# Kernel tuning notes

Hardware: AMD Instinct MI355X
Metric: run time of the kernel (lower is better)

## Reference

```python
import jax, jax.numpy as jnp
import numpy as np

N = 50000          # nodes
E = 500000         # edges (avg degree 10)
WIDTH = 128        # node feature width
HID = 128          # width * scale, scale=1 -> 2 heads of 64
HEAD = 64          # head_dim (module-level constant)
EMB = WIDTH // 2   # edge-embed width = 64
RES = 1.0
BOND = (5, 6, 2, 17)  # bond_size vocabularies


def setup_inputs() -> dict:
    key = jax.random.key(0)
    ks = jax.random.split(key, 24)
    w = lambda k, s: (jax.random.normal(k, s, jnp.float32) * 0.02)
    inp = {
        "x": jax.random.normal(ks[0], (N, WIDTH), jnp.float32),
        "edge_index": jax.random.randint(ks[1], (2, E), 0, N),
        "edge_attr": jax.random.randint(ks[2], (E, 4), 0, 3),
        # pre: Linear(width, width)
        "pre_w": w(ks[3], (WIDTH, WIDTH)), "pre_b": jnp.zeros((WIDTH,), jnp.float32),
        # msg[0..3]: Linear(width, hidden)
        "msg0_w": w(ks[4], (WIDTH, HID)), "msg0_b": jnp.zeros((HID,), jnp.float32),
        "msg1_w": w(ks[5], (WIDTH, HID)), "msg1_b": jnp.zeros((HID,), jnp.float32),
        "msg2_w": w(ks[6], (WIDTH, HID)), "msg2_b": jnp.zeros((HID,), jnp.float32),
        "msg3_w": w(ks[7], (WIDTH, HID)), "msg3_b": jnp.zeros((HID,), jnp.float32),
        # remix[0..2]: Linear(width//2, hidden)
        "remix0_w": w(ks[8], (EMB, HID)), "remix0_b": jnp.zeros((HID,), jnp.float32),
        "remix1_w": w(ks[9], (EMB, HID)), "remix1_b": jnp.zeros((HID,), jnp.float32),
        "remix2_w": w(ks[10], (EMB, HID)), "remix2_b": jnp.zeros((HID,), jnp.float32),
        # post: Linear(hidden, width)
        "post_w": w(ks[11], (HID, WIDTH)), "post_b": jnp.zeros((WIDTH,), jnp.float32),
        # EmbedBlock tables (bond_size + 1 rows each); tables 1..3 have padding_idx=0
        "emb0": w(ks[12], (BOND[0] + 1, EMB)),
        "emb1": w(ks[13], (BOND[1] + 1, EMB)).at[0].set(0.0),
        "emb2": w(ks[14], (BOND[2] + 1, EMB)).at[0].set(0.0),
        "emb3": w(ks[15], (BOND[3] + 1, EMB)).at[0].set(0.0),
        "einit": jnp.zeros((4,), jnp.float32),          # EmbedBlock.init0
        "init0": jnp.zeros((4,), jnp.float32),          # ConvBlock.init0 (hop*2+2)
    }
    return inp


def _gelu(v):
    return jax.nn.gelu(v, approximate=False)


def _ln(v):
    m = jnp.mean(v, axis=-1, keepdims=True)
    var = jnp.mean(jnp.square(v - m), axis=-1, keepdims=True)
    return (v - m) / jnp.sqrt(var + 1e-5)


def reference(x, edge_index, edge_attr, pre_w, pre_b, msg0_w, msg0_b,
              msg1_w, msg1_b, msg2_w, msg2_b, msg3_w, msg3_b,
              remix0_w, remix0_b, remix1_w, remix1_b, remix2_w, remix2_b,
              post_w, post_b, emb0, emb1, emb2, emb3, einit, init0):
    n = x.shape[0]
    e = edge_index.shape[1]
    xx = _ln(x @ pre_w + pre_b)  # pre: Linear + LayerNorm(no affine)
    # EmbedBlock: weighted sum of per-column embeddings, xw = exp(a)/sqrt(sum exp(a))
    xw = jnp.exp(einit) / jnp.sqrt(jnp.sum(jnp.exp(einit)))
    ee = (emb0[edge_attr[:, 0]] * xw[0] + emb1[edge_attr[:, 1]] * xw[1]
          + emb2[edge_attr[:, 2]] * xw[2] + emb3[edge_attr[:, 3]] * xw[3])  # [E, 64]
    src, dst = edge_index[0], edge_index[1]  # source_to_target: j=src, i=dst
    x_j = xx[src]
    x_i = xx[dst]
    scale_e = jnp.exp(init0[-2])
    scale_v = jnp.exp(init0[-1])
    q = x_i @ msg1_w + msg1_b + (ee @ remix0_w + remix0_b) * scale_e  # [E, HID]
    k = x_j @ msg2_w + msg2_b + (ee @ remix1_w + remix1_b) * scale_e
    v = _gelu(x_j @ msg3_w + msg3_b + (ee @ remix2_w + remix2_b) * scale_v)
    # per-head attention score, head_dim = 64
    att = jnp.sum((q * k).reshape(e, -1, HEAD), axis=-1, keepdims=True) / np.sqrt(HEAD)
    att = jnp.exp(att * init0[0] + init0[1])  # edge_type=0, hop=1
    msg = (v.reshape(e, -1, HEAD) * att).reshape(e, -1)  # [E, HID]
    agg = jax.ops.segment_sum(msg, dst, num_segments=n)  # scatter-add to targets
    xx = _gelu(xx @ msg0_w + msg0_b) + agg
    out = xx @ post_w + post_b
    return x + out * RES
```

## Files before the change

kernel.cpp:

```cpp
#include <hip/hip_runtime.h>
#include <cstdint>

#define WIDTH 128
#define NCOMBO 2268
#define XSL 136
#define OSL 132
#define TOTW (6 * 16384)
#define TOTU (3 * 34 * WIDTH)

typedef short bf16x8 __attribute__((ext_vector_type(8)));
typedef float f32x4  __attribute__((ext_vector_type(4)));

__device__ __forceinline__ float gelu_fast(float v) {
    float e = __builtin_amdgcn_exp2f(v * __builtin_fmaf(v * v, 0.1029437f, 2.3022081f));
    return v - v * __builtin_amdgcn_rcpf(e + 1.0f);
}
__device__ __forceinline__ short f2b(float f) {
    unsigned u = __float_as_uint(f);
    unsigned r = (u + 0x7FFFu + ((u >> 16) & 1u)) >> 16;
    return (short)r;
}
__device__ __forceinline__ float b2f_lo(unsigned u) { return __uint_as_float(u << 16); }
__device__ __forceinline__ float b2f_hi(unsigned u) { return __uint_as_float(u & 0xFFFF0000u); }
__device__ __forceinline__ unsigned pack2(float lo, float hi) {
    return (unsigned)(unsigned short)f2b(lo) | ((unsigned)(unsigned short)f2b(hi) << 16);
}

__global__ void k_f1(const float* __restrict__ einit, const float* __restrict__ init0,
                     const float* __restrict__ emb0, const float* __restrict__ emb1,
                     const float* __restrict__ emb2, const float* __restrict__ emb3,
                     const float* __restrict__ r0w, const float* __restrict__ r0b,
                     const float* __restrict__ r1w, const float* __restrict__ r1b,
                     const float* __restrict__ r2w, const float* __restrict__ r2b,
                     const float* __restrict__ pw0, const float* __restrict__ pw1,
                     const float* __restrict__ pw2, const float* __restrict__ pw3,
                     const float* __restrict__ pw4, const float* __restrict__ pw5,
                     short* __restrict__ o0, short* __restrict__ o1,
                     short* __restrict__ o2, short* __restrict__ o3,
                     short* __restrict__ o4, short* __restrict__ o5,
                     float* __restrict__ U, float* __restrict__ scal,
                     const int* __restrict__ edge_index, int* __restrict__ counts,
                     int* __restrict__ rank, int* __restrict__ done, int E) {
    int tid = blockIdx.x * blockDim.x + threadIdx.x;
    if (tid == 0) { scal[0] = init0[0]; scal[1] = init0[1]; done[0] = 0; }
    if (tid < TOTW) {
        int which = tid >> 14;
        int r = tid & 16383;
        int t    = r >> 11;
        int kc   = (r >> 9) & 3;
        int lane = (r >> 3) & 63;
        int j    = r & 7;
        int k  = kc * 32 + ((lane >> 4) << 3) + j;
        int nn = (t << 4) + (lane & 15);
        const float* w = (which == 0) ? pw0 : (which == 1) ? pw1 : (which == 2) ? pw2
                       : (which == 3) ? pw3 : (which == 4) ? pw4 : pw5;
        short* o = (which == 0) ? o0 : (which == 1) ? o1 : (which == 2) ? o2
                 : (which == 3) ? o3 : (which == 4) ? o4 : o5;
        o[r] = f2b(w[k * 128 + nn]);
    } else if (tid < TOTW + TOTU) {
        int idx = tid - TOTW;
        float e0 = expf(einit[0]), e1 = expf(einit[1]), e2 = expf(einit[2]), e3 = expf(einit[3]);
        float inv = 1.0f / sqrtf(e0 + e1 + e2 + e3);
        float xw[4] = {e0 * inv, e1 * inv, e2 * inv, e3 * inv};
        float se = expf(init0[2]);
        float sv = expf(init0[3]);
        int r   = idx / (34 * WIDTH);
        int rem = idx - r * (34 * WIDTH);
        int g   = rem / WIDTH;
        int j   = rem - g * WIDTH;
        int cc, base;
        if (g >= 16)      { cc = 3; base = 16; }
        else if (g >= 13) { cc = 2; base = 13; }
        else if (g >= 6)  { cc = 1; base = 6; }
        else              { cc = 0; base = 0; }
        int i = g - base;
        const float* em = (cc == 0) ? emb0 : (cc == 1) ? emb1 : (cc == 2) ? emb2 : emb3;
        const float* w  = (r == 0) ? r0w : (r == 1) ? r1w : r2w;
        const float* rb = (r == 0) ? r0b : (r == 1) ? r1b : r2b;
        float s = (r == 2) ? sv : se;
        float acc = 0.0f;
        const float* erow = em + i * 64;
        for (int d = 0; d < 64; ++d) acc += erow[d] * w[d * WIDTH + j];
        float val = s * xw[cc] * acc;
        if (cc == 0) val += s * rb[j];
        U[idx] = val;
    } else if (tid < TOTW + TOTU + E) {
        int e = tid - TOTW - TOTU;
        rank[e] = atomicAdd(&counts[edge_index[E + e]], 1);
    }
}

__global__ void k_f2(const int* __restrict__ counts, int* __restrict__ lscan,
                     int* __restrict__ partials, int n, int sb,
                     const float* __restrict__ U, const float* __restrict__ init0,
                     float* __restrict__ Uc, int* __restrict__ done,
                     int* __restrict__ offsets) {
    if ((int)blockIdx.x < sb) {
        __shared__ int s[256];
        __shared__ int flag;
        int t = threadIdx.x;
        int i = blockIdx.x * 256 + t;
        int v = (i < n) ? counts[i] : 0;
        s[t] = v;
        __syncthreads();
        for (int d = 1; d < 256; d <<= 1) {
            int u = (t >= d) ? s[t - d] : 0;
            __syncthreads();
            s[t] += u;
            __syncthreads();
        }
        if (i < n) lscan[i] = s[t];
        if (t == 255) atomicExch(&partials[blockIdx.x], s[255]);
        __syncthreads();
        if (t == 0) {
            __threadfence();
            flag = (atomicAdd(done, 1) == sb - 1);
        }
        __syncthreads();
        if (flag) {
            __threadfence();
            int b0 = t * 4;
            int a0 = (b0     < sb) ? partials[b0]     : 0;
            int a1 = (b0 + 1 < sb) ? partials[b0 + 1] : 0;
            int a2 = (b0 + 2 < sb) ? partials[b0 + 2] : 0;
            int a3 = (b0 + 3 < sb) ? partials[b0 + 3] : 0;
            int tsum = a0 + a1 + a2 + a3;
            __syncthreads();
            s[t] = tsum;
            __syncthreads();
            for (int d = 1; d < 256; d <<= 1) {
                int u = (t >= d) ? s[t - d] : 0;
                __syncthreads();
                s[t] += u;
                __syncthreads();
            }
            int excl = s[t] - tsum;
            if (b0     < sb) partials[b0]     = excl;
            if (b0 + 1 < sb) partials[b0 + 1] = excl + a0;
            if (b0 + 2 < sb) partials[b0 + 2] = excl + a0 + a1;
            if (b0 + 3 < sb) partials[b0 + 3] = excl + a0 + a1 + a2;
            if (t == 255) offsets[n] = s[255];
        }
    } else {
        int bi = ((int)blockIdx.x - sb) * 2 + (threadIdx.x >> 7);
        if (bi >= 3 * NCOMBO) return;
        int r  = bi / NCOMBO;
        if (r < 2 && init0[0] == 0.0f) return;
        int cb = bi - r * NCOMBO;
        int a  = cb / 378;
        int rm = cb - a * 378;
        int b  = rm / 54;
        rm -= b * 54;
        int c  = rm / 18;
        int d  = rm - c * 18;
        int j  = threadIdx.x & 127;
        const float* Ur = U + r * 34 * WIDTH;
        Uc[(size_t)bi * WIDTH + j] = Ur[a * WIDTH + j] + Ur[(6 + b) * WIDTH + j]
                                   + Ur[(13 + c) * WIDTH + j] + Ur[(16 + d) * WIDTH + j];
    }
}

__global__ void __launch_bounds__(256, 2) k_f3(
        const float* __restrict__ x,
        const short* __restrict__ preF, const float* __restrict__ pre_b,
        const short* __restrict__ w0F, const float* __restrict__ b0,
        const short* __restrict__ w1F, const float* __restrict__ b1,
        const short* __restrict__ w2F, const float* __restrict__ b2,
        const short* __restrict__ w3F, const float* __restrict__ b3,
        const float* __restrict__ scal,
        short* __restrict__ Gb, float* __restrict__ A,
        short* __restrict__ Bb, short* __restrict__ Cb, int n,
        const int* __restrict__ edge_index, const int* __restrict__ edge_attr,
        const int* __restrict__ counts, const int* __restrict__ lscan,
        const int* __restrict__ partials, const int* __restrict__ rank,
        int* __restrict__ offsets, unsigned* __restrict__ s_pk, int E,
        int gb, int eb) {
    __shared__ short xs_raw[64 * XSL];
    __shared__ short xs_xx[64 * XSL];
    int tid = threadIdx.x;

    if ((int)blockIdx.x >= gb) {
        int rb = (int)blockIdx.x - gb;
        if (rb < eb) {
            int e = rb * 256 + tid;
            if (e >= E) return;
            int src = edge_index[e];
            int dst = edge_index[E + e];
            int4 at = ((const int4*)edge_attr)[e];
            int combo = ((at.x * 7 + at.y) * 3 + at.z) * 18 + at.w;
            int off = partials[dst >> 8] + lscan[dst] - counts[dst];
            s_pk[off + rank[e]] = (unsigned)src | ((unsigned)combo << 17);
        } else {
            int i = (rb - eb) * 256 + tid;
            if (i >= n) return;
            offsets[i] = partials[i >> 8] + lscan[i] - counts[i];
        }
        return;
    }

    int w    = tid >> 6;
    int lane = tid & 63;
    int quad = lane >> 4, l16 = lane & 15;
    int m0   = blockIdx.x * 64;

    bf16x8 Bg[2][4], Bc[2][4];
#pragma unroll
    for (int tt = 0; tt < 2; ++tt)
#pragma unroll
        for (int kc = 0; kc < 4; ++kc) {
            int fo = (((2 * w + tt) * 4 + kc) * 64 + lane) * 8;
            Bg[tt][kc] = *(const bf16x8*)(w0F + fo);
            Bc[tt][kc] = *(const bf16x8*)(w3F + fo);
        }

#pragma unroll
    for (int it = 0; it < 8; ++it) {
        int fi  = it * 256 + tid;
        int row = fi >> 5, c4 = fi & 31;
        int gr  = min(m0 + row, n - 1);
        float4 v = ((const float4*)x)[(size_t)gr * 32 + c4];
        uint2 p;
        p.x = pack2(v.x, v.y);
        p.y = pack2(v.z, v.w);
        *(uint2*)(&xs_raw[row * XSL + c4 * 4]) = p;
    }
    __syncthreads();

    {
        bf16x8 a[4];
#pragma unroll
        for (int kc = 0; kc < 4; ++kc)
            a[kc] = *(const bf16x8*)(&xs_raw[(w * 16 + l16) * XSL + kc * 32 + quad * 8]);
        f32x4 acc[8];
#pragma unroll
        for (int t = 0; t < 8; ++t) acc[t] = (f32x4){0.f, 0.f, 0.f, 0.f};
#pragma unroll
        for (int kc = 0; kc < 4; ++kc)
#pragma unroll
            for (int t = 0; t < 8; ++t) {
                bf16x8 b = *(const bf16x8*)(preF + ((t * 4 + kc) * 64 + lane) * 8);
                acc[t] = __builtin_amdgcn_mfma_f32_16x16x32_bf16(a[kc], b, acc[t], 0, 0, 0);
            }
#pragma unroll
        for (int t = 0; t < 8; ++t) {
            float bv = pre_b[t * 16 + l16];
#pragma unroll
            for (int r = 0; r < 4; ++r) acc[t][r] += bv;
        }
#pragma unroll
        for (int r = 0; r < 4; ++r) {
            float s = 0.f, s2 = 0.f;
#pragma unroll
            for (int t = 0; t < 8; ++t) { float v = acc[t][r]; s += v; s2 += v * v; }
            s  += __shfl_xor(s, 1);  s2 += __shfl_xor(s2, 1);
            s  += __shfl_xor(s, 2);  s2 += __shfl_xor(s2, 2);
            s  += __shfl_xor(s, 4);  s2 += __shfl_xor(s2, 4);
            s  += __shfl_xor(s, 8);  s2 += __shfl_xor(s2, 8);
            float m   = s * (1.0f / WIDTH);
            float var = s2 * (1.0f / WIDTH) - m * m;
            float rs  = rsqrtf(var + 1e-5f);
#pragma unroll
            for (int t = 0; t < 8; ++t) acc[t][r] = (acc[t][r] - m) * rs;
        }
        int rowb = w * 16 + quad * 4;
#pragma unroll
        for (int t = 0; t < 8; ++t)
#pragma unroll
            for (int r = 0; r < 4; ++r)
                xs_xx[(rowb + r) * XSL + t * 16 + l16] = f2b(acc[t][r]);
    }
    __syncthreads();

    bf16x8 a2[4][4];
#pragma unroll
    for (int i = 0; i < 4; ++i)
#pragma unroll
        for (int kc = 0; kc < 4; ++kc)
            a2[i][kc] = *(const bf16x8*)(&xs_xx[(i * 16 + l16) * XSL + kc * 32 + quad * 8]);
    __syncthreads();

    {
        f32x4 accG[4][2], accC[4][2];
#pragma unroll
        for (int i = 0; i < 4; ++i)
#pragma unroll
            for (int tt = 0; tt < 2; ++tt) {
                accG[i][tt] = (f32x4){0.f,0.f,0.f,0.f};
                accC[i][tt] = (f32x4){0.f,0.f,0.f,0.f};
            }
#pragma unroll
        for (int kc = 0; kc < 4; ++kc)
#pragma unroll
            for (int i = 0; i < 4; ++i)
#pragma unroll
                for (int tt = 0; tt < 2; ++tt) {
                    accG[i][tt] = __builtin_amdgcn_mfma_f32_16x16x32_bf16(a2[i][kc], Bg[tt][kc], accG[i][tt], 0, 0, 0);
                    accC[i][tt] = __builtin_amdgcn_mfma_f32_16x16x32_bf16(a2[i][kc], Bc[tt][kc], accC[i][tt], 0, 0, 0);
                }
#pragma unroll
        for (int tt = 0; tt < 2; ++tt) {
            int col = (2 * w + tt) * 16 + l16;
            float bg = b0[col];
            float bc = b3[col];
#pragma unroll
            for (int i = 0; i < 4; ++i)
#pragma unroll
                for (int r = 0; r < 4; ++r) {
                    int row = i * 16 + quad * 4 + r;
                    xs_raw[row * XSL + col] = f2b(gelu_fast(accG[i][tt][r] + bg));
                    xs_xx[row * XSL + col]  = f2b(accC[i][tt][r] + bc);
                }
        }
    }
    __syncthreads();

#pragma unroll
    for (int it = 0; it < 4; ++it) {
        int si  = it * 256 + tid;
        int row = si >> 4, c8 = si & 15;
        if (m0 + row < n) {
            *(bf16x8*)(Gb + (size_t)(m0 + row) * WIDTH + c8 * 8) = *(const bf16x8*)(&xs_raw[row * XSL + c8 * 8]);
            *(bf16x8*)(Cb + (size_t)(m0 + row) * WIDTH + c8 * 8) = *(const bf16x8*)(&xs_xx[row * XSL + c8 * 8]);
        }
    }

    if (scal[0] != 0.0f) {
        bf16x8 Ba[2][4], Bbf[2][4];
#pragma unroll
        for (int tt = 0; tt < 2; ++tt)
#pragma unroll
            for (int kc = 0; kc < 4; ++kc) {
                int fo = (((2 * w + tt) * 4 + kc) * 64 + lane) * 8;
                Ba[tt][kc]  = *(const bf16x8*)(w1F + fo);
                Bbf[tt][kc] = *(const bf16x8*)(w2F + fo);
            }
        f32x4 accA[4][2], accB[4][2];
#pragma unroll
        for (int i = 0; i < 4; ++i)
#pragma unroll
            for (int tt = 0; tt < 2; ++tt) {
                accA[i][tt] = (f32x4){0.f,0.f,0.f,0.f};
                accB[i][tt] = (f32x4){0.f,0.f,0.f,0.f};
            }
#pragma unroll
        for (int kc = 0; kc < 4; ++kc)
#pragma unroll
            for (int i = 0; i < 4; ++i)
#pragma unroll
                for (int tt = 0; tt < 2; ++tt) {
                    accA[i][tt] = __builtin_amdgcn_mfma_f32_16x16x32_bf16(a2[i][kc], Ba[tt][kc],  accA[i][tt], 0, 0, 0);
                    accB[i][tt] = __builtin_amdgcn_mfma_f32_16x16x32_bf16(a2[i][kc], Bbf[tt][kc], accB[i][tt], 0, 0, 0);
                }
#pragma unroll
        for (int tt = 0; tt < 2; ++tt) {
            int col = (2 * w + tt) * 16 + l16;
            float ba = b1[col];
            float bb = b2[col];
#pragma unroll
            for (int i = 0; i < 4; ++i)
#pragma unroll
                for (int r = 0; r < 4; ++r) {
                    int row = m0 + i * 16 + quad * 4 + r;
                    if (row < n) {
                        size_t idx = (size_t)row * WIDTH + col;
                        A[idx]  = accA[i][tt][r] + ba;
                        Bb[idx] = f2b(accB[i][tt][r] + bb);
                    }
                }
        }
    }
}

__global__ void __launch_bounds__(256)
k_agg(const int* __restrict__ offsets, const unsigned* __restrict__ s_pk,
      const float* __restrict__ A, const short* __restrict__ Bb,
      const short* __restrict__ Cb, const float* __restrict__ Uc,
      const float* __restrict__ scal, const short* __restrict__ Gb,
      short* __restrict__ hb, int n) {
    int wid = threadIdx.x >> 6;
    int L   = threadIdx.x & 63;
    int node = blockIdx.x * 4 + wid;
    if (node >= n) return;
    int start = __builtin_amdgcn_readfirstlane(offsets[node]);
    int end   = __builtin_amdgcn_readfirstlane(offsets[node + 1]);

    const unsigned* Cb32 = (const unsigned*)Cb;
    const unsigned* Bb32 = (const unsigned*)Bb;
    const float2* U0c2 = (const float2*)(Uc);
    const float2* U1c2 = (const float2*)(Uc + (size_t)NCOMBO * WIDTH);
    const float2* U2c2 = (const float2*)(Uc + 2 * (size_t)NCOMBO * WIDTH);

    float i0 = scal[0], i1 = scal[1];
    float acc0 = 0.0f, acc1 = 0.0f;

    if (i0 == 0.0f) {
        int p = start;
        for (; p + 4 <= end; p += 4) {
            unsigned pk0 = __builtin_amdgcn_readfirstlane(s_pk[p]);
            unsigned pk1 = __builtin_amdgcn_readfirstlane(s_pk[p + 1]);
            unsigned pk2 = __builtin_amdgcn_readfirstlane(s_pk[p + 2]);
            unsigned pk3 = __builtin_amdgcn_readfirstlane(s_pk[p + 3]);
            const unsigned* cp0 = Cb32 + ((size_t)(pk0 & 0x1FFFFu) << 6);
            const unsigned* cp1 = Cb32 + ((size_t)(pk1 & 0x1FFFFu) << 6);
            const unsigned* cp2 = Cb32 + ((size_t)(pk2 & 0x1FFFFu) << 6);
            const unsigned* cp3 = Cb32 + ((size_t)(pk3 & 0x1FFFFu) << 6);
            const float2* up0 = U2c2 + ((size_t)(pk0 >> 17) << 6);
            const float2* up1 = U2c2 + ((size_t)(pk1 >> 17) << 6);
            const float2* up2 = U2c2 + ((size_t)(pk2 >> 17) << 6);
            const float2* up3 = U2c2 + ((size_t)(pk3 >> 17) << 6);
            unsigned cc0 = cp0[L], cc1 = cp1[L], cc2 = cp2[L], cc3 = cp3[L];
            float2   uu0 = up0[L], uu1 = up1[L], uu2 = up2[L], uu3 = up3[L];
            acc0 += gelu_fast(b2f_lo(cc0) + uu0.x);
            acc1 += gelu_fast(b2f_hi(cc0) + uu0.y);
            acc0 += gelu_fast(b2f_lo(cc1) + uu1.x);
            acc1 += gelu_fast(b2f_hi(cc1) + uu1.y);
            acc0 += gelu_fast(b2f_lo(cc2) + uu2.x);
            acc1 += gelu_fast(b2f_hi(cc2) + uu2.y);
            acc0 += gelu_fast(b2f_lo(cc3) + uu3.x);
            acc1 += gelu_fast(b2f_hi(cc3) + uu3.y);
        }
        if (p + 2 <= end) {
            unsigned pk0 = __builtin_amdgcn_readfirstlane(s_pk[p]);
            unsigned pk1 = __builtin_amdgcn_readfirstlane(s_pk[p + 1]);
            const unsigned* cp0 = Cb32 + ((size_t)(pk0 & 0x1FFFFu) << 6);
            const unsigned* cp1 = Cb32 + ((size_t)(pk1 & 0x1FFFFu) << 6);
            const float2* up0 = U2c2 + ((size_t)(pk0 >> 17) << 6);
            const float2* up1 = U2c2 + ((size_t)(pk1 >> 17) << 6);
            unsigned cc0 = cp0[L], cc1 = cp1[L];
            float2   uu0 = up0[L], uu1 = up1[L];
            acc0 += gelu_fast(b2f_lo(cc0) + uu0.x);
            acc1 += gelu_fast(b2f_hi(cc0) + uu0.y);
            acc0 += gelu_fast(b2f_lo(cc1) + uu1.x);
            acc1 += gelu_fast(b2f_hi(cc1) + uu1.y);
            p += 2;
        }
        if (p < end) {
            unsigned pk0 = __builtin_amdgcn_readfirstlane(s_pk[p]);
            const unsigned* cp0 = Cb32 + ((size_t)(pk0 & 0x1FFFFu) << 6);
            const float2* up0 = U2c2 + ((size_t)(pk0 >> 17) << 6);
            unsigned cc0 = cp0[L];
            float2   uu0 = up0[L];
            acc0 += gelu_fast(b2f_lo(cc0) + uu0.x);
            acc1 += gelu_fast(b2f_hi(cc0) + uu0.y);
        }
        float sE = __expf(i1);
        acc0 *= sE; acc1 *= sE;
    } else {
        float2 av = *(const float2*)(A + (size_t)node * WIDTH + 2 * L);
        int p = start;
        for (; p + 2 <= end; p += 2) {
            unsigned pk0 = s_pk[p], pk1 = s_pk[p + 1];
            unsigned sA = pk0 & 0x1FFFFu, cA = pk0 >> 17;
            unsigned sB = pk1 & 0x1FFFFu, cB = pk1 >> 17;
            float2 u0a = U0c2[cA * 64 + L], u0b = U0c2[cB * 64 + L];
            float2 u1a = U1c2[cA * 64 + L], u1b = U1c2[cB * 64 + L];
            float2 u2a = U2c2[cA * 64 + L], u2b = U2c2[cB * 64 + L];
            unsigned bba = Bb32[sA * 64 + L], bbb = Bb32[sB * 64 + L];
            unsigned cca = Cb32[sA * 64 + L], ccb = Cb32[sB * 64 + L];
            {
                float q0 = av.x + u0a.x, q1 = av.y + u0a.y;
                float k0 = b2f_lo(bba) + u1a.x, k1 = b2f_hi(bba) + u1a.y;
                float v0 = gelu_fast(b2f_lo(cca) + u2a.x);
                float v1 = gelu_fast(b2f_hi(cca) + u2a.y);
                float s = q0 * k0 + q1 * k1;
                s += __shfl_xor(s, 1);
                s += __shfl_xor(s, 2);
                s += __shfl_xor(s, 4);
                s += __shfl_xor(s, 8);
                s += __shfl_xor(s, 16);
                float att = __expf(s * 0.125f * i0 + i1);
                acc0 += v0 * att;
                acc1 += v1 * att;
            }
            {
                float q0 = av.x + u0b.x, q1 = av.y + u0b.y;
                float k0 = b2f_lo(bbb) + u1b.x, k1 = b2f_hi(bbb) + u1b.y;
                float v0 = gelu_fast(b2f_lo(ccb) + u2b.x);
                float v1 = gelu_fast(b2f_hi(ccb) + u2b.y);
                float s = q0 * k0 + q1 * k1;
                s += __shfl_xor(s, 1);
                s += __shfl_xor(s, 2);
                s += __shfl_xor(s, 4);
                s += __shfl_xor(s, 8);
                s += __shfl_xor(s, 16);
                float att = __expf(s * 0.125f * i0 + i1);
                acc0 += v0 * att;
                acc1 += v1 * att;
            }
        }
        if (p < end) {
            unsigned pk = s_pk[p];
            unsigned sA = pk & 0x1FFFFu, cA = pk >> 17;
            float2 u0 = U0c2[cA * 64 + L];
            float2 u1 = U1c2[cA * 64 + L];
            float2 u2 = U2c2[cA * 64 + L];
            unsigned bb = Bb32[sA * 64 + L];
            unsigned cc = Cb32[sA * 64 + L];
            float q0 = av.x + u0.x, q1 = av.y + u0.y;
            float k0 = b2f_lo(bb) + u1.x, k1 = b2f_hi(bb) + u1.y;
            float v0 = gelu_fast(b2f_lo(cc) + u2.x);
            float v1 = gelu_fast(b2f_hi(cc) + u2.y);
            float s = q0 * k0 + q1 * k1;
            s += __shfl_xor(s, 1);
            s += __shfl_xor(s, 2);
            s += __shfl_xor(s, 4);
            s += __shfl_xor(s, 8);
            s += __shfl_xor(s, 16);
            float att = __expf(s * 0.125f * i0 + i1);
            acc0 += v0 * att;
            acc1 += v1 * att;
        }
    }
    unsigned g = ((const unsigned*)Gb)[(size_t)node * 64 + L];
    ((unsigned*)hb)[(size_t)node * 64 + L] = pack2(b2f_lo(g) + acc0, b2f_hi(g) + acc1);
}

__global__ void __launch_bounds__(256, 2) k_post(
        const float* __restrict__ x, const short* __restrict__ hb,
        const short* __restrict__ postF, const float* __restrict__ post_b,
        float* __restrict__ out, int n) {
    __shared__ short hs[64 * XSL];
    __shared__ float os[64 * OSL];
    int tid  = threadIdx.x;
    int w    = tid >> 6;
    int lane = tid & 63;
    int quad = lane >> 4, l16 = lane & 15;
    int m0   = blockIdx.x * 64;

    bf16x8 Bp[2][4];
#pragma unroll
    for (int tt = 0; tt < 2; ++tt)
#pragma unroll
        for (int kc = 0; kc < 4; ++kc)
            Bp[tt][kc] = *(const bf16x8*)(postF + (((2 * w + tt) * 4 + kc) * 64 + lane) * 8);

#pragma unroll
    for (int it = 0; it < 4; ++it) {
        int si  = it * 256 + tid;
        int row = si >> 4, c8 = si & 15;
        int gr  = min(m0 + row, n - 1);
        *(bf16x8*)(&hs[row * XSL + c8 * 8]) = *(const bf16x8*)(hb + (size_t)gr * WIDTH + c8 * 8);
    }
    __syncthreads();

    bf16x8 a[4][4];
#pragma unroll
    for (int i = 0; i < 4; ++i)
#pragma unroll
        for (int kc = 0; kc < 4; ++kc)
            a[i][kc] = *(const bf16x8*)(&hs[(i * 16 + l16) * XSL + kc * 32 + quad * 8]);

    f32x4 acc[4][2];
#pragma unroll
    for (int i = 0; i < 4; ++i)
#pragma unroll
        for (int tt = 0; tt < 2; ++tt) acc[i][tt] = (f32x4){0.f,0.f,0.f,0.f};
#pragma unroll
    for (int kc = 0; kc < 4; ++kc)
#pragma unroll
        for (int i = 0; i < 4; ++i)
#pragma unroll
            for (int tt = 0; tt < 2; ++tt)
                acc[i][tt] = __builtin_amdgcn_mfma_f32_16x16x32_bf16(a[i][kc], Bp[tt][kc], acc[i][tt], 0, 0, 0);

#pragma unroll
    for (int tt = 0; tt < 2; ++tt) {
        int col = (2 * w + tt) * 16 + l16;
        float bv = post_b[col];
#pragma unroll
        for (int i = 0; i < 4; ++i)
#pragma unroll
            for (int r = 0; r < 4; ++r)
                os[(i * 16 + quad * 4 + r) * OSL + col] = acc[i][tt][r] + bv;
    }
    __syncthreads();

#pragma unroll
    for (int it = 0; it < 8; ++it) {
        int fi  = it * 256 + tid;
        int row = fi >> 5, c4 = fi & 31;
        if (m0 + row < n) {
            float4 xv = ((const float4*)x)[(size_t)(m0 + row) * 32 + c4];
            float4 av = *(const float4*)(&os[row * OSL + c4 * 4]);
            float4 ov = {xv.x + av.x, xv.y + av.y, xv.z + av.z, xv.w + av.w};
            ((float4*)out)[(size_t)(m0 + row) * 32 + c4] = ov;
        }
    }
}

extern "C" void kernel_launch(void* const* d_in, const int* in_sizes, int n_in,
                              void* d_out, int out_size, void* d_ws, size_t ws_size,
                              hipStream_t stream) {
    const float* x      = (const float*)d_in[0];
    const int*   eidx   = (const int*)d_in[1];
    const int*   eattr  = (const int*)d_in[2];
    const float* pre_w  = (const float*)d_in[3];
    const float* pre_b  = (const float*)d_in[4];
    const float* msg0_w = (const float*)d_in[5];
    const float* msg0_b = (const float*)d_in[6];
    const float* msg1_w = (const float*)d_in[7];
    const float* msg1_b = (const float*)d_in[8];
    const float* msg2_w = (const float*)d_in[9];
    const float* msg2_b = (const float*)d_in[10];
    const float* msg3_w = (const float*)d_in[11];
    const float* msg3_b = (const float*)d_in[12];
    const float* r0w    = (const float*)d_in[13];
    const float* r0b    = (const float*)d_in[14];
    const float* r1w    = (const float*)d_in[15];
    const float* r1b    = (const float*)d_in[16];
    const float* r2w    = (const float*)d_in[17];
    const float* r2b    = (const float*)d_in[18];
    const float* post_w = (const float*)d_in[19];
    const float* post_b = (const float*)d_in[20];
    const float* emb0   = (const float*)d_in[21];
    const float* emb1   = (const float*)d_in[22];
    const float* emb2   = (const float*)d_in[23];
    const float* emb3   = (const float*)d_in[24];
    const float* einit  = (const float*)d_in[25];
    const float* init0  = (const float*)d_in[26];

    int n = in_sizes[0] / WIDTH;
    int E = in_sizes[2] / 4;
    size_t NW = (size_t)n * WIDTH;

    float* ws   = (float*)d_ws;
    float* A    = ws;
    float* U    = ws + NW;
    float* Uc   = U + 3 * 34 * WIDTH;
    float* scal = Uc + 3 * (size_t)NCOMBO * WIDTH;
    short* sw   = (short*)(scal + 2);
    short* preF  = sw;
    short* w0F   = sw + 16384;
    short* w1F   = sw + 2 * 16384;
    short* w2F   = sw + 3 * 16384;
    short* w3F   = sw + 4 * 16384;
    short* postF = sw + 5 * 16384;
    short* Bb    = sw + 6 * 16384;
    short* Cb    = Bb + NW;
    short* Gb    = Cb + NW;
    short* hb    = Gb + NW;
    int*      ib       = (int*)(hb + NW);
    int*      offsets  = ib;
    int*      counts   = offsets + (n + 1);
    int*      lscan    = counts + n;
    int*      partials = lscan + n;
    int*      rank     = partials + 1024;
    unsigned* s_pk     = (unsigned*)(rank + E);
    int*      done     = (int*)(s_pk + E);

    hipMemsetAsync(counts, 0, (size_t)n * sizeof(int), stream);

    int f1_total = TOTW + TOTU + E;
    k_f1<<<(f1_total + 255) / 256, 256, 0, stream>>>(
        einit, init0, emb0, emb1, emb2, emb3,
        r0w, r0b, r1w, r1b, r2w, r2b,
        pre_w, msg0_w, msg1_w, msg2_w, msg3_w, post_w,
        preF, w0F, w1F, w2F, w3F, postF, U, scal,
        eidx, counts, rank, done, E);

    int sb  = (n + 255) / 256;
    int pcb = (3 * NCOMBO + 1) / 2;
    k_f2<<<sb + pcb, 256, 0, stream>>>(counts, lscan, partials, n, sb, U, init0, Uc,
                                       done, offsets);

    int gb = (n + 63) / 64;
    int eb = (E + 255) / 256;
    k_f3<<<gb + eb + sb, 256, 0, stream>>>(
        x, preF, pre_b, w0F, msg0_b, w1F, msg1_b, w2F, msg2_b, w3F, msg3_b,
        scal, Gb, A, Bb, Cb, n,
        eidx, eattr, counts, lscan, partials, rank, offsets, s_pk, E, gb, eb);

    k_agg<<<(n + 3) / 4, 256, 0, stream>>>(offsets, s_pk, A, Bb, Cb, Uc, scal, Gb, hb, n);
    k_post<<<gb, 256, 0, stream>>>(x, hb, postF, post_b, (float*)d_out, n);
}
```

Baseline: 232.9 us.

## Fuse edge aggregation into post projection kernel via shared-memory tile

Merges the per-node aggregation kernel and the post linear kernel into one kernel. Each 512-thread block aggregates 32 nodes (four per wave) into a bf16 tile in LDS, then runs the MFMA post projection and residual add directly on it. This removes the hb global round trip and one launch. It also loads edge descriptors 64 at a time with one vector load and reads them with readlane instead of per-edge scalar loads. In exchange, each wave walks four nodes in sequence, blocks wait at a barrier for their slowest node, and post weights are reloaded per block with smaller MFMA tiles.

```diff
diff --git a/kernel.cpp b/kernel.cpp
--- a/kernel.cpp
+++ b/kernel.cpp
@@ -371,213 +371,139 @@
     }
 }
 
-__global__ void __launch_bounds__(256)
-k_agg(const int* __restrict__ offsets, const unsigned* __restrict__ s_pk,
-      const float* __restrict__ A, const short* __restrict__ Bb,
-      const short* __restrict__ Cb, const float* __restrict__ Uc,
-      const float* __restrict__ scal, const short* __restrict__ Gb,
-      short* __restrict__ hb, int n) {
-    int wid = threadIdx.x >> 6;
-    int L   = threadIdx.x & 63;
-    int node = blockIdx.x * 4 + wid;
-    if (node >= n) return;
-    int start = __builtin_amdgcn_readfirstlane(offsets[node]);
-    int end   = __builtin_amdgcn_readfirstlane(offsets[node + 1]);
+__global__ void __launch_bounds__(512, 6)
+k_ap(const int* __restrict__ offsets, const unsigned* __restrict__ s_pk,
+     const float* __restrict__ A, const short* __restrict__ Bb,
+     const short* __restrict__ Cb, const float* __restrict__ Uc,
+     const float* __restrict__ scal, const short* __restrict__ Gb,
+     const float* __restrict__ x, const short* __restrict__ postF,
+     const float* __restrict__ post_b, float* __restrict__ out, int n) {
+    __shared__ short hs[32 * XSL];
+    __shared__ float os[32 * OSL];
+    int tid = threadIdx.x;
+    int w   = tid >> 6;
+    int L   = tid & 63;
+    int m0  = blockIdx.x * 32;
 
     const unsigned* Cb32 = (const unsigned*)Cb;
     const unsigned* Bb32 = (const unsigned*)Bb;
     const float2* U0c2 = (const float2*)(Uc);
     const float2* U1c2 = (const float2*)(Uc + (size_t)NCOMBO * WIDTH);
     const float2* U2c2 = (const float2*)(Uc + 2 * (size_t)NCOMBO * WIDTH);
+    unsigned* hs32 = (unsigned*)hs;
 
     float i0 = scal[0], i1 = scal[1];
-    float acc0 = 0.0f, acc1 = 0.0f;
-
-    if (i0 == 0.0f) {
-        int p = start;
-        for (; p + 4 <= end; p += 4) {
-            unsigned pk0 = __builtin_amdgcn_readfirstlane(s_pk[p]);
-            unsigned pk1 = __builtin_amdgcn_readfirstlane(s_pk[p + 1]);
-            unsigned pk2 = __builtin_amdgcn_readfirstlane(s_pk[p + 2]);
-            unsigned pk3 = __builtin_amdgcn_readfirstlane(s_pk[p + 3]);
-            const unsigned* cp0 = Cb32 + ((size_t)(pk0 & 0x1FFFFu) << 6);
-            const unsigned* cp1 = Cb32 + ((size_t)(pk1 & 0x1FFFFu) << 6);
-            const unsigned* cp2 = Cb32 + ((size_t)(pk2 & 0x1FFFFu) << 6);
-            const unsigned* cp3 = Cb32 + ((size_t)(pk3 & 0x1FFFFu) << 6);
-            const float2* up0 = U2c2 + ((size_t)(pk0 >> 17) << 6);
-            const float2* up1 = U2c2 + ((size_t)(pk1 >> 17) << 6);
-            const float2* up2 = U2c2 + ((size_t)(pk2 >> 17) << 6);
-            const float2* up3 = U2c2 + ((size_t)(pk3 >> 17) << 6);
-            unsigned cc0 = cp0[L], cc1 = cp1[L], cc2 = cp2[L], cc3 = cp3[L];
-            float2   uu0 = up0[L], uu1 = up1[L], uu2 = up2[L], uu3 = up3[L];
-            acc0 += gelu_fast(b2f_lo(cc0) + uu0.x);
-            acc1 += gelu_fast(b2f_hi(cc0) + uu0.y);
-            acc0 += gelu_fast(b2f_lo(cc1) + uu1.x);
-            acc1 += gelu_fast(b2f_hi(cc1) + uu1.y);
-            acc0 += gelu_fast(b2f_lo(cc2) + uu2.x);
-            acc1 += gelu_fast(b2f_hi(cc2) + uu2.y);
-            acc0 += gelu_fast(b2f_lo(cc3) + uu3.x);
-            acc1 += gelu_fast(b2f_hi(cc3) + uu3.y);
-        }
-        if (p + 2 <= end) {
-            unsigned pk0 = __builtin_amdgcn_readfirstlane(s_pk[p]);
-            unsigned pk1 = __builtin_amdgcn_readfirstlane(s_pk[p + 1]);
-            const unsigned* cp0 = Cb32 + ((size_t)(pk0 & 0x1FFFFu) << 6);
-            const unsigned* cp1 = Cb32 + ((size_t)(pk1 & 0x1FFFFu) << 6);
-            const float2* up0 = U2c2 + ((size_t)(pk0 >> 17) << 6);
-            const float2* up1 = U2c2 + ((size_t)(pk1 >> 17) << 6);
-            unsigned cc0 = cp0[L], cc1 = cp1[L];
-            float2   uu0 = up0[L], uu1 = up1[L];
-            acc0 += gelu_fast(b2f_lo(cc0) + uu0.x);
-            acc1 += gelu_fast(b2f_hi(cc0) + uu0.y);
-            acc0 += gelu_fast(b2f_lo(cc1) + uu1.x);
-            acc1 += gelu_fast(b2f_hi(cc1) + uu1.y);
-            p += 2;
-        }
-        if (p < end) {
-            unsigned pk0 = __builtin_amdgcn_readfirstlane(s_pk[p]);
-            const unsigned* cp0 = Cb32 + ((size_t)(pk0 & 0x1FFFFu) << 6);
-            const float2* up0 = U2c2 + ((size_t)(pk0 >> 17) << 6);
-            unsigned cc0 = cp0[L];
-            float2   uu0 = up0[L];
-            acc0 += gelu_fast(b2f_lo(cc0) + uu0.x);
-            acc1 += gelu_fast(b2f_hi(cc0) + uu0.y);
-        }
-        float sE = __expf(i1);
-        acc0 *= sE; acc1 *= sE;
-    } else {
-        float2 av = *(const float2*)(A + (size_t)node * WIDTH + 2 * L);
-        int p = start;
-        for (; p + 2 <= end; p += 2) {
-            unsigned pk0 = s_pk[p], pk1 = s_pk[p + 1];
-            unsigned sA = pk0 & 0x1FFFFu, cA = pk0 >> 17;
-            unsigned sB = pk1 & 0x1FFFFu, cB = pk1 >> 17;
-            float2 u0a = U0c2[cA * 64 + L], u0b = U0c2[cB * 64 + L];
-            float2 u1a = U1c2[cA * 64 + L], u1b = U1c2[cB * 64 + L];
-            float2 u2a = U2c2[cA * 64 + L], u2b = U2c2[cB * 64 + L];
-            unsigned bba = Bb32[sA * 64 + L], bbb = Bb32[sB * 64 + L];
-            unsigned cca = Cb32[sA * 64 + L], ccb = Cb32[sB * 64 + L];
-            {
-                float q0 = av.x + u0a.x, q1 = av.y + u0a.y;
-                float k0 = b2f_lo(bba) + u1a.x, k1 = b2f_hi(bba) + u1a.y;
-                float v0 = gelu_fast(b2f_lo(cca) + u2a.x);
-                float v1 = gelu_fast(b2f_hi(cca) + u2a.y);
-                float s = q0 * k0 + q1 * k1;
-                s += __shfl_xor(s, 1);
-                s += __shfl_xor(s, 2);
-                s += __shfl_xor(s, 4);
-                s += __shfl_xor(s, 8);
-                s += __shfl_xor(s, 16);
-                float att = __expf(s * 0.125f * i0 + i1);
-                acc0 += v0 * att;
-                acc1 += v1 * att;
+    float sE = __expf(i1);
+
+    for (int k = 0; k < 4; ++k) {
+        int row  = w * 4 + k;
+        int node = m0 + row;
+        float acc0 = 0.0f, acc1 = 0.0f;
+        if (node < n) {
+            int start = __builtin_amdgcn_readfirstlane(offsets[node]);
+            int end   = __builtin_amdgcn_readfirstlane(offsets[node + 1]);
+            if (i0 == 0.0f) {
+                for (int base = start; base < end; base += 64) {
+                    int cnt = min(end - base, 64);
+                    unsigned pkv = (L < cnt) ? s_pk[base + L] : 0u;
+                    int i = 0;
+                    for (; i + 4 <= cnt; i += 4) {
+                        unsigned pk0 = __builtin_amdgcn_readlane(pkv, i);
+                        unsigned pk1 = __builtin_amdgcn_readlane(pkv, i + 1);
+                        unsigned pk2 = __builtin_amdgcn_readlane(pkv, i + 2);
+                        unsigned pk3 = __builtin_amdgcn_readlane(pkv, i + 3);
+                        const unsigned* cp0 = Cb32 + ((size_t)(pk0 & 0x1FFFFu) << 6);
+                        const unsigned* cp1 = Cb32 + ((size_t)(pk1 & 0x1FFFFu) << 6);
+                        const unsigned* cp2 = Cb32 + ((size_t)(pk2 & 0x1FFFFu) << 6);
+                        const unsigned* cp3 = Cb32 + ((size_t)(pk3 & 0x1FFFFu) << 6);
+                        const float2* up0 = U2c2 + ((size_t)(pk0 >> 17) << 6);
+                        const float2* up1 = U2c2 + ((size_t)(pk1 >> 17) << 6);
+                        const float2* up2 = U2c2 + ((size_t)(pk2 >> 17) << 6);
+                        const float2* up3 = U2c2 + ((size_t)(pk3 >> 17) << 6);
+                        unsigned cc0 = cp0[L], cc1 = cp1[L], cc2 = cp2[L], cc3 = cp3[L];
+                        float2   uu0 = up0[L], uu1 = up1[L], uu2 = up2[L], uu3 = up3[L];
+                        acc0 += gelu_fast(b2f_lo(cc0) + uu0.x);
+                        acc1 += gelu_fast(b2f_hi(cc0) + uu0.y);
+                        acc0 += gelu_fast(b2f_lo(cc1) + uu1.x);
+                        acc1 += gelu_fast(b2f_hi(cc1) + uu1.y);
+                        acc0 += gelu_fast(b2f_lo(cc2) + uu2.x);
+                        acc1 += gelu_fast(b2f_hi(cc2) + uu2.y);
+                        acc0 += gelu_fast(b2f_lo(cc3) + uu3.x);
+                        acc1 += gelu_fast(b2f_hi(cc3) + uu3.y);
+                    }
+                    for (; i < cnt; ++i) {
+                        unsigned pk0 = __builtin_amdgcn_readlane(pkv, i);
+                        const unsigned* cp0 = Cb32 + ((size_t)(pk0 & 0x1FFFFu) << 6);
+                        const float2* up0 = U2c2 + ((size_t)(pk0 >> 17) << 6);
+                        unsigned cc0 = cp0[L];
+                        float2   uu0 = up0[L];
+                        acc0 += gelu_fast(b2f_lo(cc0) + uu0.x);
+                        acc1 += gelu_fast(b2f_hi(cc0) + uu0.y);
+                    }
+                }
+                acc0 *= sE; acc1 *= sE;
+            } else {
+                float2 av = *(const float2*)(A + (size_t)node * WIDTH + 2 * L);
+                for (int p = start; p < end; ++p) {
+                    unsigned pk = s_pk[p];
+                    unsigned sA = pk & 0x1FFFFu, cA = pk >> 17;
+                    float2 u0 = U0c2[cA * 64 + L];
+                    float2 u1 = U1c2[cA * 64 + L];
+                    float2 u2 = U2c2[cA * 64 + L];
+                    unsigned bb = Bb32[sA * 64 + L];
+                    unsigned cc = Cb32[sA * 64 + L];
+                    float q0 = av.x + u0.x, q1 = av.y + u0.y;
+                    float k0 = b2f_lo(bb) + u1.x, k1 = b2f_hi(bb) + u1.y;
+                    float v0 = gelu_fast(b2f_lo(cc) + u2.x);
+                    float v1 = gelu_fast(b2f_hi(cc) + u2.y);
+                    float s = q0 * k0 + q1 * k1;
+                    s += __shfl_xor(s, 1);
+                    s += __shfl_xor(s, 2);
+                    s += __shfl_xor(s, 4);
+                    s += __shfl_xor(s, 8);
+                    s += __shfl_xor(s, 16);
+                    float att = __expf(s * 0.125f * i0 + i1);
+                    acc0 += v0 * att;
+                    acc1 += v1 * att;
+                }
             }
-            {
-                float q0 = av.x + u0b.x, q1 = av.y + u0b.y;
-                float k0 = b2f_lo(bbb) + u1b.x, k1 = b2f_hi(bbb) + u1b.y;
-                float v0 = gelu_fast(b2f_lo(ccb) + u2b.x);
-                float v1 = gelu_fast(b2f_hi(ccb) + u2b.y);
-                float s = q0 * k0 + q1 * k1;
-                s += __shfl_xor(s, 1);
-                s += __shfl_xor(s, 2);
-                s += __shfl_xor(s, 4);
-                s += __shfl_xor(s, 8);
-                s += __shfl_xor(s, 16);
-                float att = __expf(s * 0.125f * i0 + i1);
-                acc0 += v0 * att;
-                acc1 += v1 * att;
-            }
-        }
-        if (p < end) {
-            unsigned pk = s_pk[p];
-            unsigned sA = pk & 0x1FFFFu, cA = pk >> 17;
-            float2 u0 = U0c2[cA * 64 + L];
-            float2 u1 = U1c2[cA * 64 + L];
-            float2 u2 = U2c2[cA * 64 + L];
-            unsigned bb = Bb32[sA * 64 + L];
-            unsigned cc = Cb32[sA * 64 + L];
-            float q0 = av.x + u0.x, q1 = av.y + u0.y;
-            float k0 = b2f_lo(bb) + u1.x, k1 = b2f_hi(bb) + u1.y;
-            float v0 = gelu_fast(b2f_lo(cc) + u2.x);
-            float v1 = gelu_fast(b2f_hi(cc) + u2.y);
-            float s = q0 * k0 + q1 * k1;
-            s += __shfl_xor(s, 1);
-            s += __shfl_xor(s, 2);
-            s += __shfl_xor(s, 4);
-            s += __shfl_xor(s, 8);
-            s += __shfl_xor(s, 16);
-            float att = __expf(s * 0.125f * i0 + i1);
-            acc0 += v0 * att;
-            acc1 += v1 * att;
-        }
-    }
-    unsigned g = ((const unsigned*)Gb)[(size_t)node * 64 + L];
-    ((unsigned*)hb)[(size_t)node * 64 + L] = pack2(b2f_lo(g) + acc0, b2f_hi(g) + acc1);
-}
-
-__global__ void __launch_bounds__(256, 2) k_post(
-        const float* __restrict__ x, const short* __restrict__ hb,
-        const short* __restrict__ postF, const float* __restrict__ post_b,
-        float* __restrict__ out, int n) {
-    __shared__ short hs[64 * XSL];
-    __shared__ float os[64 * OSL];
-    int tid  = threadIdx.x;
-    int w    = tid >> 6;
-    int lane = tid & 63;
-    int quad = lane >> 4, l16 = lane & 15;
-    int m0   = blockIdx.x * 64;
-
-    bf16x8 Bp[2][4];
-#pragma unroll
-    for (int tt = 0; tt < 2; ++tt)
-#pragma unroll
-        for (int kc = 0; kc < 4; ++kc)
-            Bp[tt][kc] = *(const bf16x8*)(postF + (((2 * w + tt) * 4 + kc) * 64 + lane) * 8);
-
-#pragma unroll
-    for (int it = 0; it < 4; ++it) {
-        int si  = it * 256 + tid;
-        int row = si >> 4, c8 = si & 15;
-        int gr  = min(m0 + row, n - 1);
-        *(bf16x8*)(&hs[row * XSL + c8 * 8]) = *(const bf16x8*)(hb + (size_t)gr * WIDTH + c8 * 8);
+            unsigned g = ((const unsigned*)Gb)[(size_t)node * 64 + L];
+            hs32[row * (XSL / 2) + L] = pack2(b2f_lo(g) + acc0, b2f_hi(g) + acc1);
+        } else {
+            hs32[row * (XSL / 2) + L] = 0u;
+        }
     }
     __syncthreads();
 
-    bf16x8 a[4][4];
-#pragma unroll
-    for (int i = 0; i < 4; ++i)
-#pragma unroll
-        for (int kc = 0; kc < 4; ++kc)
-            a[i][kc] = *(const bf16x8*)(&hs[(i * 16 + l16) * XSL + kc * 32 + quad * 8]);
-
-    f32x4 acc[4][2];
-#pragma unroll
-    for (int i = 0; i < 4; ++i)
-#pragma unroll
-        for (int tt = 0; tt < 2; ++tt) acc[i][tt] = (f32x4){0.f,0.f,0.f,0.f};
+    int quad = L >> 4, l16 = L & 15;
+    int ri    = w & 1;
+    int cpair = w >> 1;
+
+    bf16x8 a[4];
 #pragma unroll
     for (int kc = 0; kc < 4; ++kc)
-#pragma unroll
-        for (int i = 0; i < 4; ++i)
-#pragma unroll
-            for (int tt = 0; tt < 2; ++tt)
-                acc[i][tt] = __builtin_amdgcn_mfma_f32_16x16x32_bf16(a[i][kc], Bp[tt][kc], acc[i][tt], 0, 0, 0);
+        a[kc] = *(const bf16x8*)(&hs[(ri * 16 + l16) * XSL + kc * 32 + quad * 8]);
 
 #pragma unroll
     for (int tt = 0; tt < 2; ++tt) {
-        int col = (2 * w + tt) * 16 + l16;
+        int t = cpair * 2 + tt;
+        f32x4 acc = (f32x4){0.f, 0.f, 0.f, 0.f};
+#pragma unroll
+        for (int kc = 0; kc < 4; ++kc) {
+            bf16x8 b = *(const bf16x8*)(postF + ((t * 4 + kc) * 64 + L) * 8);
+            acc = __builtin_amdgcn_mfma_f32_16x16x32_bf16(a[kc], b, acc, 0, 0, 0);
+        }
+        int col = t * 16 + l16;
         float bv = post_b[col];
 #pragma unroll
-        for (int i = 0; i < 4; ++i)
-#pragma unroll
-            for (int r = 0; r < 4; ++r)
-                os[(i * 16 + quad * 4 + r) * OSL + col] = acc[i][tt][r] + bv;
+        for (int r = 0; r < 4; ++r)
+            os[(ri * 16 + quad * 4 + r) * OSL + col] = acc[r] + bv;
     }
     __syncthreads();
 
 #pragma unroll
-    for (int it = 0; it < 8; ++it) {
-        int fi  = it * 256 + tid;
+    for (int it = 0; it < 2; ++it) {
+        int fi  = it * 512 + tid;
         int row = fi >> 5, c4 = fi & 31;
         if (m0 + row < n) {
             float4 xv = ((const float4*)x)[(size_t)(m0 + row) * 32 + c4];
@@ -638,8 +564,7 @@
     short* Bb    = sw + 6 * 16384;
     short* Cb    = Bb + NW;
     short* Gb    = Cb + NW;
-    short* hb    = Gb + NW;
-    int*      ib       = (int*)(hb + NW);
+    int*      ib       = (int*)(Gb + NW);
     int*      offsets  = ib;
     int*      counts   = offsets + (n + 1);
     int*      lscan    = counts + n;
@@ -670,6 +595,6 @@
         scal, Gb, A, Bb, Cb, n,
         eidx, eattr, counts, lscan, partials, rank, offsets, s_pk, E, gb, eb);
 
-    k_agg<<<(n + 3) / 4, 256, 0, stream>>>(offsets, s_pk, A, Bb, Cb, Uc, scal, Gb, hb, n);
-    k_post<<<gb, 256, 0, stream>>>(x, hb, postF, post_b, (float*)d_out, n);
-}
+    k_ap<<<(n + 31) / 32, 512, 0, stream>>>(offsets, s_pk, A, Bb, Cb, Uc, scal, Gb,
+                                            x, postF, post_b, (float*)d_out, n);
+}
```

Measured after the change: 234.1 us. Within noise of the previous version (+0.5%).
